# Performance work log

Measured on AMD Instinct MI355X. Metric: run time of the kernel, lower is better.

The kernel has to match this reference:

```python
import jax, jax.numpy as jnp
import numpy as np
import math

MID = 48       # mid_channels
HEADS = 4      # num_heads
POS = 16       # mid_channels // 3 (row/col positional channels)


def _unfold(x, p):
    """nn.Unfold with kernel p, padding p//2: (..., H, W) -> (..., p, p, H, W)."""
    H, W = x.shape[-2], x.shape[-1]
    pad = p // 2
    xp = jnp.pad(x, [(0, 0)] * (x.ndim - 2) + [(pad, pad), (pad, pad)])
    return jnp.stack(
        [jnp.stack([xp[..., k:k + H, l:l + W] for l in range(p)], axis=-3)
         for k in range(p)], axis=-4)


def _pe_mlp(idx, w1, b1, g, b, w2, b2):
    """Conv2d(1->16,1x1) -> LayerNorm(16) -> Swish -> Conv2d(16->POS,1x1) on scalar coords."""
    t = idx.reshape(-1, 1)                         # (N,1)
    h = t @ w1.T + b1                              # (N,16)
    mu = jnp.mean(h, -1, keepdims=True)
    var = jnp.var(h, -1, keepdims=True)
    h = (h - mu) * jax.lax.rsqrt(var + 1e-5) * g + b
    h = h * jax.nn.sigmoid(h)                      # Swish
    e = h @ w2.T + b2                              # (N,POS)
    return e.reshape(idx.shape + (e.shape[-1],))   # (V,P,P,POS)


def setup_inputs() -> dict:
    key = jax.random.key(0)
    ks = jax.random.split(key, 32)
    B, Cin, G, H, W, P, Cout = 2, 32, 4, 28, 28, 7, 64

    def n(k, shp, s=0.05):
        return jax.random.normal(k, shp, dtype=jnp.float32) * s

    inp = {"x": jax.random.normal(ks[0], (B, Cin, G, H, W), dtype=jnp.float32)}
    inp["Wq"] = n(ks[1], (MID * HEADS, Cin)); inp["bq"] = n(ks[2], (MID * HEADS,))
    inp["Wk"] = n(ks[3], (MID * HEADS, Cin)); inp["bk"] = n(ks[4], (MID * HEADS,))
    inp["Wv"] = n(ks[5], (MID * HEADS, Cin)); inp["bv"] = n(ks[6], (MID * HEADS,))
    inp["Wout"] = n(ks[7], (Cout, MID * HEADS)); inp["bout"] = n(ks[8], (Cout,))
    inp["row_w1"] = n(ks[9], (16, 1)); inp["row_b1"] = n(ks[10], (16,))
    inp["row_ln_g"] = jnp.ones((16,), jnp.float32); inp["row_ln_b"] = jnp.zeros((16,), jnp.float32)
    inp["row_w2"] = n(ks[11], (POS, 16)); inp["row_b2"] = n(ks[12], (POS,))
    inp["col_w1"] = n(ks[13], (16, 1)); inp["col_b1"] = n(ks[14], (16,))
    inp["col_ln_g"] = jnp.ones((16,), jnp.float32); inp["col_ln_b"] = jnp.zeros((16,), jnp.float32)
    inp["col_w2"] = n(ks[15], (POS, 16)); inp["col_b2"] = n(ks[16], (POS,))
    inp["group_emb"] = n(ks[17], (G, MID - 2 * POS))
    # rotated relative spatial positions, normalized to [-1, 1]
    lin = np.linspace(-1.0, 1.0, P).astype(np.float32)
    r = np.repeat(lin[:, None], P, 1)
    c = np.repeat(lin[None, :], P, 0)
    rows, cols = [], []
    for v in range(G):
        th = v * math.pi / 2.0
        rows.append(math.cos(th) * r - math.sin(th) * c)
        cols.append(math.sin(th) * r + math.cos(th) * c)
    inp["row_indices"] = jnp.asarray(np.stack(rows, 0))
    inp["col_indices"] = jnp.asarray(np.stack(cols, 0))
    # acted relative group positions for cyclic group C4
    ar = np.arange(G)
    gi = (ar[:, None, None] + ar[None, None, :] - ar[None, :, None]) % G
    inp["g_indices"] = jnp.asarray(gi, dtype=jnp.int32)
    return inp


def _forward(x, Wq, bq, Wk, bk, Wv, bv, Wout, bout,
             row_w1, row_b1, row_ln_g, row_ln_b, row_w2, row_b2,
             col_w1, col_b1, col_ln_g, col_ln_b, col_w2, col_b2,
             group_emb, row_indices, col_indices, g_indices):
    B, Cin, G, H, W = x.shape
    P = row_indices.shape[-1]
    sqn = jnp.sqrt(jnp.float32(Cin))

    def proj(Wm, bm):  # 1x1 Conv3d -> (B, MID, HEADS, G, H, W)
        y = jnp.einsum('oi,bigyx->bogyx', Wm, x) + bm[None, :, None, None, None]
        return y.reshape(B, MID, HEADS, G, H, W)

    q = proj(Wq, bq)
    k = proj(Wk, bk)
    v = proj(Wv, bv)
    k_loc = _unfold(k, P)   # (B, MID, HEADS, G, P, P, H, W)
    v_loc = _unfold(v, P)

    content = jnp.einsum('bchgij,bchmklij->bhgijmkl', q, k_loc)
    row_e = _pe_mlp(row_indices, row_w1, row_b1, row_ln_g, row_ln_b, row_w2, row_b2)
    col_e = _pe_mlp(col_indices, col_w1, col_b1, col_ln_g, col_ln_b, col_w2, col_b2)
    row_s = jnp.einsum('bchgij,vklc->bhvgijkl', q[:, :POS], row_e)
    col_s = jnp.einsum('bchgij,vklc->bhvgijkl', q[:, POS:2 * POS], col_e)
    g_e = group_emb[g_indices]                              # (V, G, M, gdim)
    g_s = jnp.einsum('bchgij,vgmc->bhvgijm', q[:, 2 * POS:], g_e)

    # scores: (b, h, v, g, i, j, m, k, l)
    scores = (row_s[:, :, :, :, :, :, None] + col_s[:, :, :, :, :, :, None]
              + g_s[..., None, None] + content[:, :, None]) / sqn

    # mask patch positions that fall outside the image (-inf -> prob 0)
    valid = _unfold(jnp.ones((H, W), jnp.float32), P)       # (P, P, H, W)
    valid = jnp.transpose(valid, (2, 3, 0, 1))[None, None, None, None, :, :, None, :, :]
    scores = jnp.where(valid > 0.5, scores, -jnp.inf)

    shp = scores.shape
    probs = jax.nn.softmax(scores.reshape(shp[:-3] + (-1,)), axis=-1).reshape(shp)

    o = jnp.einsum('bhvgijmkl,bchmklij->bchvij', probs, v_loc)  # (B, MID, HEADS, V, H, W)
    o = o.reshape(B, MID * HEADS, G, H, W)
    return jnp.einsum('oi,bivyx->bovyx', Wout, o) + bout[None, :, None, None, None]


def reference(x, Wq, bq, Wk, bk, Wv, bv, Wout, bout,
              row_w1, row_b1, row_ln_g, row_ln_b, row_w2, row_b2,
              col_w1, col_b1, col_ln_g, col_ln_b, col_w2, col_b2,
              group_emb, row_indices, col_indices, g_indices):
    return _forward(x, Wq, bq, Wk, bk, Wv, bv, Wout, bout,
                    row_w1, row_b1, row_ln_g, row_ln_b, row_w2, row_b2,
                    col_w1, col_b1, col_ln_g, col_ln_b, col_w2, col_b2,
                    group_emb, row_indices, col_indices, g_indices)
```

## Files before the change

### kernel.cpp

```cpp
#include <hip/hip_runtime.h>
#include <math.h>

#define Bb   2
#define CIN  32
#define Gg   4
#define NH   4
#define Hh   28
#define Ww   28
#define HW   784
#define Pp   7
#define PP   49
#define MID  48
#define COUT 64
#define OC   192

#define QOFF  0
#define KOFF  1204224
#define VOFF  2408448
#define OOFF  3612672

#define INV_SQN 0.17677669529663687f

__device__ unsigned g_peT2[Gg * 16 * PP];
__device__ unsigned g_geT2[8 * 64];
__device__ float    g_WT2[OC * COUT];

typedef _Float16 h2f __attribute__((ext_vector_type(2)));

__device__ __forceinline__ unsigned packh2(float a, float b) {
    auto r = __builtin_amdgcn_cvt_pkrtz(a, b);
    return __builtin_bit_cast(unsigned, r);
}

__device__ __forceinline__ float fdot2(unsigned a, unsigned b, float c) {
    return __builtin_amdgcn_fdot2(__builtin_bit_cast(h2f, a),
                                  __builtin_bit_cast(h2f, b), c, false);
}

__global__ __launch_bounds__(192) void qkvpe_kernel(const float* __restrict__ x,
    const float* __restrict__ Wq, const float* __restrict__ bq,
    const float* __restrict__ Wk, const float* __restrict__ bk,
    const float* __restrict__ Wv, const float* __restrict__ bv,
    const float* row_w1, const float* row_b1,
    const float* row_g,  const float* row_bb,
    const float* row_w2, const float* row_b2,
    const float* col_w1, const float* col_b1,
    const float* col_g,  const float* col_bb,
    const float* col_w2, const float* col_b2,
    const float* row_idx, const float* col_idx,
    const float* group_emb, const int* g_indices,
    const float* Wout,
    float* __restrict__ ws)
{
    int tid = threadIdx.x;
    if (blockIdx.x == Bb * Gg * Hh * 2) {
        for (int t = tid; t < 2 * Gg * PP; t += 192) {
            int half = t / (Gg * PP);
            int n    = t - half * (Gg * PP);
            int v = n / PP, kl = n % PP;
            const float* w1 = half ? col_w1 : row_w1;
            const float* b1 = half ? col_b1 : row_b1;
            const float* lg = half ? col_g  : row_g;
            const float* lb = half ? col_bb : row_bb;
            const float* w2 = half ? col_w2 : row_w2;
            const float* b2 = half ? col_b2 : row_b2;
            float tv = half ? col_idx[n] : row_idx[n];

            float hb[16];
            float mean = 0.f;
            for (int k = 0; k < 16; k++) { hb[k] = tv * w1[k] + b1[k]; mean += hb[k]; }
            mean *= (1.f / 16.f);
            float var = 0.f;
            for (int k = 0; k < 16; k++) { float d = hb[k] - mean; var += d * d; }
            var *= (1.f / 16.f);
            float inv = 1.f / sqrtf(var + 1e-5f);
            for (int k = 0; k < 16; k++) {
                float hn = (hb[k] - mean) * inv * lg[k] + lb[k];
                hb[k] = hn / (1.f + expf(-hn));
            }
            float accv[16];
            for (int p = 0; p < 16; p++) {
                float acc = b2[p];
                for (int k = 0; k < 16; k++) acc += hb[k] * w2[p * 16 + k];
                accv[p] = acc * INV_SQN;
            }
            for (int i2 = 0; i2 < 8; i2++)
                g_peT2[(v * 16 + half * 8 + i2) * PP + kl] =
                    packh2(accv[2 * i2], accv[2 * i2 + 1]);
        }
        for (int t = tid; t < 64; t += 192) {
            int gi = g_indices[t];
            for (int i2 = 0; i2 < 8; i2++)
                g_geT2[i2 * 64 + t] = packh2(group_emb[gi * 16 + 2 * i2] * INV_SQN,
                                             group_emb[gi * 16 + 2 * i2 + 1] * INV_SQN);
        }
        for (int idx = tid; idx < OC * COUT; idx += 192) {
            int tp = idx >> 6, o = idx & 63;
            int h = tp / MID, c = tp % MID;
            g_WT2[idx] = Wout[o * OC + c * NH + h];
        }
        return;
    }

    __shared__ float xs[CIN * 16];
    int r = blockIdx.x;
    int jh = r & 1; r >>= 1;
    int i = r % Hh; r /= Hh;
    int g = r & 3;  int b = r >> 2;
    int j0 = jh * 14;

    for (int idx = tid; idx < CIN * 14; idx += 192) {
        int ci = idx / 14, jj = idx % 14;
        xs[ci * 16 + jj] = x[((b * CIN + ci) * Gg + g) * HW + i * Ww + j0 + jj];
    }
    __syncthreads();

    int h = tid / MID, c = tid % MID;
    int oo = c * NH + h;
    int wbase = (((b * NH + h) * Gg + g) * HW + i * Ww + j0) * MID + c;

    const float* Wm[3]  = {Wq, Wk, Wv};
    const float* bm[3]  = {bq, bk, bv};
    const int    off[3] = {QOFF, KOFF, VOFF};
    const float  scl[3] = {1.0f, INV_SQN, 1.0f};
    for (int p = 0; p < 3; p++) {
        const float4* Wr4 = (const float4*)(Wm[p] + oo * CIN);
        float bias = bm[p][oo];
        float a[14];
        #pragma unroll
        for (int j = 0; j < 14; j++) a[j] = bias;

        #pragma unroll 2
        for (int ci8 = 0; ci8 < 8; ci8++) {
            float4 wv4 = Wr4[ci8];
            int cb = ci8 * 4;
#define CHAN(WV, CI)                                                          \
            {                                                                 \
                float wv = WV;                                                \
                float4 xA = *(const float4*)&xs[(CI) * 16 + 0];               \
                float4 xB = *(const float4*)&xs[(CI) * 16 + 4];               \
                float4 xC = *(const float4*)&xs[(CI) * 16 + 8];               \
                float2 xD = *(const float2*)&xs[(CI) * 16 + 12];              \
                a[0] += wv * xA.x;  a[1] += wv * xA.y;                        \
                a[2] += wv * xA.z;  a[3] += wv * xA.w;                        \
                a[4] += wv * xB.x;  a[5] += wv * xB.y;                        \
                a[6] += wv * xB.z;  a[7] += wv * xB.w;                        \
                a[8] += wv * xC.x;  a[9] += wv * xC.y;                        \
                a[10] += wv * xC.z; a[11] += wv * xC.w;                       \
                a[12] += wv * xD.x; a[13] += wv * xD.y;                       \
            }
            CHAN(wv4.x, cb + 0)
            CHAN(wv4.y, cb + 1)
            CHAN(wv4.z, cb + 2)
            CHAN(wv4.w, cb + 3)
#undef CHAN
        }
        float s = scl[p];
        #pragma unroll
        for (int j = 0; j < 14; j++) ws[off[p] + wbase + j * MID] = a[j] * s;
    }
}

__global__ __launch_bounds__(256, 4) void attn_kernel(float* __restrict__ ws)
{
    __shared__ unsigned kvb[7280];
    __shared__ __align__(16) unsigned pp2[4][PP][8];
    __shared__ __align__(16) unsigned qp[4][4][26];
    __shared__ float gsm[4][64];

    const int tid  = threadIdx.x;
    const int wave = tid >> 6;
    const int lane = tid & 63;

    int blk = blockIdx.x;
    int j0 = (blk % 7) * 4;
    int i  = (blk / 7) % Hh;
    int bh = blk / (7 * Hh);
    int b = bh >> 2, h = bh & 3;
    int j  = j0 + wave;
    int ij = i * Ww + j;

    const float* Qt  = ws + QOFF;
    const float* Kbh = ws + KOFF + (size_t)bh * Gg * HW * MID;
    const float* Vbh = ws + VOFF + (size_t)bh * Gg * HW * MID;
    float* Ot = ws + OOFF;

    if (lane < 48) {
        int g = lane / 12, c4 = lane % 12;
        float4 qv = *(const float4*)&Qt[((size_t)(bh * Gg + g) * HW + ij) * MID + c4 * 4];
        qp[wave][g][c4 * 2]     = packh2(qv.x, qv.y);
        qp[wave][g][c4 * 2 + 1] = packh2(qv.z, qv.w);
    }

    for (int t = tid; t < 3360; t += 256) {
        int c4 = t % 12; int cell = (t / 12) % 70; int m = t / 840;
        int gy = i - 3 + cell / 10, gx = j0 - 3 + cell % 10;
        float4 val = {0.f, 0.f, 0.f, 0.f};
        if ((unsigned)gy < Hh && (unsigned)gx < Ww)
            val = *(const float4*)&Kbh[((size_t)(m * HW + gy * Ww + gx)) * MID + c4 * 4];
        *(uint2*)&kvb[(m * 70 + cell) * 26 + c4 * 2] = make_uint2(packh2(val.x, val.y),
                                                                  packh2(val.z, val.w));
    }

    int kk = lane / Pp, ll = lane % Pp;
    int cell = (lane < PP) ? kk * 10 + ll + wave : 0;
    bool vmask = (lane < PP) && ((unsigned)(i + kk - 3) < Hh) && ((unsigned)(j + ll - 3) < Ww);
    int lclamp = lane < PP ? lane : 0;

    float per[4][4] = {};
    #pragma unroll 2
    for (int u = 0; u < 16; u++) {
        unsigned q0 = qp[wave][0][u], q1 = qp[wave][1][u];
        unsigned q2 = qp[wave][2][u], q3 = qp[wave][3][u];
        #pragma unroll
        for (int v = 0; v < 4; v++) {
            unsigned pk = g_peT2[(v * 16 + u) * PP + lclamp];
            per[v][0] = fdot2(pk, q0, per[v][0]);
            per[v][1] = fdot2(pk, q1, per[v][1]);
            per[v][2] = fdot2(pk, q2, per[v][2]);
            per[v][3] = fdot2(pk, q3, per[v][3]);
        }
    }

    {
        int g = (lane >> 2) & 3;
        float ga = 0.f;
        #pragma unroll
        for (int u = 0; u < 8; u++)
            ga = fdot2(g_geT2[u * 64 + lane], qp[wave][g][16 + u], ga);
        gsm[wave][lane] = ga;
    }
    __syncthreads();

    float acc[4][4] = {};
    #pragma unroll 2
    for (int u2 = 0; u2 < 12; u2++) {
        uint2 qg0 = *(const uint2*)&qp[wave][0][u2 * 2];
        uint2 qg1 = *(const uint2*)&qp[wave][1][u2 * 2];
        uint2 qg2 = *(const uint2*)&qp[wave][2][u2 * 2];
        uint2 qg3 = *(const uint2*)&qp[wave][3][u2 * 2];
        #pragma unroll
        for (int m = 0; m < 4; m++) {
            uint2 kp = *(const uint2*)&kvb[(m * 70 + cell) * 26 + u2 * 2];
            acc[m][0] = fdot2(kp.x, qg0.x, acc[m][0]);
            acc[m][0] = fdot2(kp.y, qg0.y, acc[m][0]);
            acc[m][1] = fdot2(kp.x, qg1.x, acc[m][1]);
            acc[m][1] = fdot2(kp.y, qg1.y, acc[m][1]);
            acc[m][2] = fdot2(kp.x, qg2.x, acc[m][2]);
            acc[m][2] = fdot2(kp.y, qg2.y, acc[m][2]);
            acc[m][3] = fdot2(kp.x, qg3.x, acc[m][3]);
            acc[m][3] = fdot2(kp.y, qg3.y, acc[m][3]);
        }
    }

    float ppr[4][4] = {};
    #pragma unroll
    for (int v = 0; v < 4; v++) {
        #pragma unroll
        for (int g = 0; g < 4; g++) {
            int vg = v * 4 + g;
            float ex[4]; float ls = 0.f;
            #pragma unroll
            for (int m = 0; m < 4; m++) {
                float sv = acc[m][g] + per[v][g] + gsm[wave][vg * 4 + m];
                ex[m] = vmask ? __expf(sv) : 0.f;
                ls += ex[m];
            }
            #pragma unroll
            for (int d = 32; d > 0; d >>= 1) ls += __shfl_xor(ls, d, 64);
            float rinv = 1.0f / ls;
            #pragma unroll
            for (int m = 0; m < 4; m++) ppr[v][m] += ex[m] * rinv;
        }
    }
    if (lane < PP) {
        uint4 w0, w1;
        w0.x = packh2(ppr[0][0], ppr[0][1]); w0.y = packh2(ppr[0][2], ppr[0][3]);
        w0.z = packh2(ppr[1][0], ppr[1][1]); w0.w = packh2(ppr[1][2], ppr[1][3]);
        w1.x = packh2(ppr[2][0], ppr[2][1]); w1.y = packh2(ppr[2][2], ppr[2][3]);
        w1.z = packh2(ppr[3][0], ppr[3][1]); w1.w = packh2(ppr[3][2], ppr[3][3]);
        *(uint4*)&pp2[wave][lane][0] = w0;
        *(uint4*)&pp2[wave][lane][4] = w1;
    }
    __syncthreads();

    {
        _Float16* vh = (_Float16*)kvb;
        for (int t = tid; t < 3360; t += 256) {
            int c4 = t % 12; int cl = (t / 12) % 70; int m = t / 840;
            int gy = i - 3 + cl / 10, gx = j0 - 3 + cl % 10;
            float4 val = {0.f, 0.f, 0.f, 0.f};
            if ((unsigned)gy < Hh && (unsigned)gx < Ww)
                val = *(const float4*)&Vbh[((size_t)(m * HW + gy * Ww + gx)) * MID + c4 * 4];
            int hb2 = (cl * 48 + c4 * 4) * 4 + m;
            vh[hb2]      = (_Float16)val.x;
            vh[hb2 + 4]  = (_Float16)val.y;
            vh[hb2 + 8]  = (_Float16)val.z;
            vh[hb2 + 12] = (_Float16)val.w;
        }
    }
    __syncthreads();

    if (lane < MID) {
        float o0 = 0.f, o1 = 0.f, o2 = 0.f, o3 = 0.f;
        #pragma unroll 2
        for (int kl2 = 0; kl2 < PP; kl2++) {
            int cell2 = (kl2 / 7) * 10 + (kl2 % 7) + wave;
            uint2 vv = *(const uint2*)&kvb[(cell2 * 48 + lane) * 2];
            uint2 pa = *(const uint2*)&pp2[wave][kl2][0];
            uint2 pb = *(const uint2*)&pp2[wave][kl2][2];
            uint2 pc = *(const uint2*)&pp2[wave][kl2][4];
            uint2 pd = *(const uint2*)&pp2[wave][kl2][6];
            o0 = fdot2(vv.x, pa.x, o0); o0 = fdot2(vv.y, pa.y, o0);
            o1 = fdot2(vv.x, pb.x, o1); o1 = fdot2(vv.y, pb.y, o1);
            o2 = fdot2(vv.x, pc.x, o2); o2 = fdot2(vv.y, pc.y, o2);
            o3 = fdot2(vv.x, pd.x, o3); o3 = fdot2(vv.y, pd.y, o3);
        }
        Ot[((size_t)(b * Gg + 0) * HW + ij) * OC + h * MID + lane] = o0;
        Ot[((size_t)(b * Gg + 1) * HW + ij) * OC + h * MID + lane] = o1;
        Ot[((size_t)(b * Gg + 2) * HW + ij) * OC + h * MID + lane] = o2;
        Ot[((size_t)(b * Gg + 3) * HW + ij) * OC + h * MID + lane] = o3;
    }
}

__global__ __launch_bounds__(256) void outproj_kernel(const float* __restrict__ bout,
                                                      const float* __restrict__ ws,
                                                      float* __restrict__ out)
{
    __shared__ float ov[16 * 193];
    __shared__ float res[64 * 17];
    int tid = threadIdx.x;
    int p0 = blockIdx.x * 16;
    const float* Ot = ws + OOFF;

    for (int idx = tid; idx < 16 * OC; idx += 256) {
        int pl = idx / OC, t = idx % OC;
        ov[pl * 193 + t] = Ot[(size_t)(p0 + pl) * OC + t];
    }
    __syncthreads();

    int o = tid & 63, pg = tid >> 6;
    float a0 = bout[o], a1 = a0, a2 = a0, a3 = a0;
    for (int t = 0; t < OC; t++) {
        float w = g_WT2[t * 64 + o];
        a0 += w * ov[(pg     ) * 193 + t];
        a1 += w * ov[(pg +  4) * 193 + t];
        a2 += w * ov[(pg +  8) * 193 + t];
        a3 += w * ov[(pg + 12) * 193 + t];
    }
    res[o * 17 + pg     ] = a0;
    res[o * 17 + pg +  4] = a1;
    res[o * 17 + pg +  8] = a2;
    res[o * 17 + pg + 12] = a3;
    __syncthreads();

    for (int idx = tid; idx < 1024; idx += 256) {
        int o2 = idx >> 4, pl = idx & 15;
        int p = p0 + pl;
        int ij2 = p % HW; int bv = p / HW; int v = bv & 3; int bb = bv >> 2;
        out[((bb * COUT + o2) * Gg + v) * HW + ij2] = res[o2 * 17 + pl];
    }
}

extern "C" void kernel_launch(void* const* d_in, const int* in_sizes, int n_in,
                              void* d_out, int out_size, void* d_ws, size_t ws_size,
                              hipStream_t stream)
{
    const float* x      = (const float*)d_in[0];
    const float* Wq     = (const float*)d_in[1];
    const float* bq     = (const float*)d_in[2];
    const float* Wk     = (const float*)d_in[3];
    const float* bk     = (const float*)d_in[4];
    const float* Wv     = (const float*)d_in[5];
    const float* bv     = (const float*)d_in[6];
    const float* Wout   = (const float*)d_in[7];
    const float* bout   = (const float*)d_in[8];
    const float* row_w1 = (const float*)d_in[9];
    const float* row_b1 = (const float*)d_in[10];
    const float* row_g  = (const float*)d_in[11];
    const float* row_bb = (const float*)d_in[12];
    const float* row_w2 = (const float*)d_in[13];
    const float* row_b2 = (const float*)d_in[14];
    const float* col_w1 = (const float*)d_in[15];
    const float* col_b1 = (const float*)d_in[16];
    const float* col_g  = (const float*)d_in[17];
    const float* col_bb = (const float*)d_in[18];
    const float* col_w2 = (const float*)d_in[19];
    const float* col_b2 = (const float*)d_in[20];
    const float* gemb   = (const float*)d_in[21];
    const float* ridx   = (const float*)d_in[22];
    const float* cidx   = (const float*)d_in[23];
    const int*   gidx   = (const int*)d_in[24];

    float* ws  = (float*)d_ws;
    float* out = (float*)d_out;

    qkvpe_kernel<<<Bb * Gg * Hh * 2 + 1, 192, 0, stream>>>(
        x, Wq, bq, Wk, bk, Wv, bv,
        row_w1, row_b1, row_g, row_bb, row_w2, row_b2,
        col_w1, col_b1, col_g, col_bb, col_w2, col_b2,
        ridx, cidx, gemb, gidx, Wout, ws);
    attn_kernel<<<Bb * NH * Hh * (Ww / 4), 256, 0, stream>>>(ws);
    outproj_kernel<<<Bb * Gg * HW / 16, 256, 0, stream>>>(bout, ws, out);
}
```

Baseline: 202.6 us.

## Pad K smem stride, repack V tile as uint4, transpose Wout via smem

Changes the K tile row stride in shared memory from 26 to 27 words to reduce LDS bank conflicts in the QK dot loop. Rewrites the V staging so each thread loads two group slices and writes one packed uint4 with a plane-major layout, replacing scattered 16-bit stores. The V reads in the PV loop become two 32-bit loads instead of one 64-bit load. The Wout transpose in the setup block now goes through a padded shared tile for coalesced global access, at the cost of extra barriers and shared memory in every qkv block.

```diff
diff --git a/kernel.cpp b/kernel.cpp
--- a/kernel.cpp
+++ b/kernel.cpp
@@ -52,6 +52,8 @@
     const float* Wout,
     float* __restrict__ ws)
 {
+    __shared__ float xs[CIN * 16];
+    __shared__ float wtmp[16 * 193];
     int tid = threadIdx.x;
     if (blockIdx.x == Bb * Gg * Hh * 2) {
         for (int t = tid; t < 2 * Gg * PP; t += 192) {
@@ -94,15 +96,23 @@
                 g_geT2[i2 * 64 + t] = packh2(group_emb[gi * 16 + 2 * i2] * INV_SQN,
                                              group_emb[gi * 16 + 2 * i2 + 1] * INV_SQN);
         }
-        for (int idx = tid; idx < OC * COUT; idx += 192) {
-            int tp = idx >> 6, o = idx & 63;
-            int h = tp / MID, c = tp % MID;
-            g_WT2[idx] = Wout[o * OC + c * NH + h];
+        for (int chunk = 0; chunk < 4; chunk++) {
+            int obase = chunk * 16;
+            __syncthreads();
+            for (int idx = tid; idx < 16 * OC; idx += 192) {
+                int ol = idx / OC, t = idx % OC;
+                wtmp[ol * 193 + t] = Wout[(obase + ol) * OC + t];
+            }
+            __syncthreads();
+            for (int idx = tid; idx < 16 * OC; idx += 192) {
+                int tp = idx / 16, ol = idx % 16;
+                int h = tp / MID, c = tp % MID;
+                g_WT2[tp * 64 + obase + ol] = wtmp[ol * 193 + c * NH + h];
+            }
         }
         return;
     }
 
-    __shared__ float xs[CIN * 16];
     int r = blockIdx.x;
     int jh = r & 1; r >>= 1;
     int i = r % Hh; r /= Hh;
@@ -163,7 +173,7 @@
 
 __global__ __launch_bounds__(256, 4) void attn_kernel(float* __restrict__ ws)
 {
-    __shared__ unsigned kvb[7280];
+    __shared__ __align__(16) unsigned kvb[7560];
     __shared__ __align__(16) unsigned pp2[4][PP][8];
     __shared__ __align__(16) unsigned qp[4][4][26];
     __shared__ float gsm[4][64];
@@ -198,7 +208,7 @@
         float4 val = {0.f, 0.f, 0.f, 0.f};
         if ((unsigned)gy < Hh && (unsigned)gx < Ww)
             val = *(const float4*)&Kbh[((size_t)(m * HW + gy * Ww + gx)) * MID + c4 * 4];
-        *(uint2*)&kvb[(m * 70 + cell) * 26 + c4 * 2] = make_uint2(packh2(val.x, val.y),
+        *(uint2*)&kvb[(m * 70 + cell) * 27 + c4 * 2] = make_uint2(packh2(val.x, val.y),
                                                                   packh2(val.z, val.w));
     }
 
@@ -241,7 +251,7 @@
         uint2 qg3 = *(const uint2*)&qp[wave][3][u2 * 2];
         #pragma unroll
         for (int m = 0; m < 4; m++) {
-            uint2 kp = *(const uint2*)&kvb[(m * 70 + cell) * 26 + u2 * 2];
+            uint2 kp = *(const uint2*)&kvb[(m * 70 + cell) * 27 + u2 * 2];
             acc[m][0] = fdot2(kp.x, qg0.x, acc[m][0]);
             acc[m][0] = fdot2(kp.y, qg0.y, acc[m][0]);
             acc[m][1] = fdot2(kp.x, qg1.x, acc[m][1]);
@@ -284,20 +294,19 @@
     }
     __syncthreads();
 
-    {
-        _Float16* vh = (_Float16*)kvb;
-        for (int t = tid; t < 3360; t += 256) {
-            int c4 = t % 12; int cl = (t / 12) % 70; int m = t / 840;
-            int gy = i - 3 + cl / 10, gx = j0 - 3 + cl % 10;
-            float4 val = {0.f, 0.f, 0.f, 0.f};
-            if ((unsigned)gy < Hh && (unsigned)gx < Ww)
-                val = *(const float4*)&Vbh[((size_t)(m * HW + gy * Ww + gx)) * MID + c4 * 4];
-            int hb2 = (cl * 48 + c4 * 4) * 4 + m;
-            vh[hb2]      = (_Float16)val.x;
-            vh[hb2 + 4]  = (_Float16)val.y;
-            vh[hb2 + 8]  = (_Float16)val.z;
-            vh[hb2 + 12] = (_Float16)val.w;
-        }
+    for (int t = tid; t < 1680; t += 256) {
+        int c4 = t % 12; int cl = (t / 12) % 70; int p = t / 840;
+        int gy = i - 3 + cl / 10, gx = j0 - 3 + cl % 10;
+        float4 va = {0.f, 0.f, 0.f, 0.f}, vb = {0.f, 0.f, 0.f, 0.f};
+        if ((unsigned)gy < Hh && (unsigned)gx < Ww) {
+            const float* vp = &Vbh[((size_t)((2 * p) * HW + gy * Ww + gx)) * MID + c4 * 4];
+            va = *(const float4*)vp;
+            vb = *(const float4*)(vp + HW * MID);
+        }
+        uint4 w;
+        w.x = packh2(va.x, vb.x); w.y = packh2(va.y, vb.y);
+        w.z = packh2(va.z, vb.z); w.w = packh2(va.w, vb.w);
+        *(uint4*)&kvb[(p * 70 + cl) * 48 + c4 * 4] = w;
     }
     __syncthreads();
 
@@ -306,15 +315,16 @@
         #pragma unroll 2
         for (int kl2 = 0; kl2 < PP; kl2++) {
             int cell2 = (kl2 / 7) * 10 + (kl2 % 7) + wave;
-            uint2 vv = *(const uint2*)&kvb[(cell2 * 48 + lane) * 2];
+            unsigned v01 = kvb[cell2 * 48 + lane];
+            unsigned v23 = kvb[(70 + cell2) * 48 + lane];
             uint2 pa = *(const uint2*)&pp2[wave][kl2][0];
             uint2 pb = *(const uint2*)&pp2[wave][kl2][2];
             uint2 pc = *(const uint2*)&pp2[wave][kl2][4];
             uint2 pd = *(const uint2*)&pp2[wave][kl2][6];
-            o0 = fdot2(vv.x, pa.x, o0); o0 = fdot2(vv.y, pa.y, o0);
-            o1 = fdot2(vv.x, pb.x, o1); o1 = fdot2(vv.y, pb.y, o1);
-            o2 = fdot2(vv.x, pc.x, o2); o2 = fdot2(vv.y, pc.y, o2);
-            o3 = fdot2(vv.x, pd.x, o3); o3 = fdot2(vv.y, pd.y, o3);
+            o0 = fdot2(v01, pa.x, o0); o0 = fdot2(v23, pa.y, o0);
+            o1 = fdot2(v01, pb.x, o1); o1 = fdot2(v23, pb.y, o1);
+            o2 = fdot2(v01, pc.x, o2); o2 = fdot2(v23, pc.y, o2);
+            o3 = fdot2(v01, pd.x, o3); o3 = fdot2(v23, pd.y, o3);
         }
         Ot[((size_t)(b * Gg + 0) * HW + ij) * OC + h * MID + lane] = o0;
         Ot[((size_t)(b * Gg + 1) * HW + ij) * OC + h * MID + lane] = o1;
```

New measurement: 190.9 us. 5.8% less time.
